# Kernel optimization log

Measured on AMD Instinct MI355X. Metric: run time of the kernel, lower is better.

Reference implementation:

```python
import jax, jax.numpy as jnp
import numpy as np

K = 1024            # atoms per chain
L = 4 * K - 9       # 2*(K-3) sin/cos dihedrals + (K-2) len13 + (K-1) bond lengths
EPS = 1e-6


def _denorm(v, lo, hi):
    # map [-1, 1] -> [lo, hi]
    return (v + 1.0) * 0.5 * (hi - lo) + lo


def _output_arr2values(v):
    # split flat NN output into (sin/cos dihedrals, hedron len13, bond lengths)
    n_d = K - 3
    sc = v[: 2 * n_d].reshape(n_d, 2)                     # (sin, cos) per dihedral
    d13 = _denorm(v[2 * n_d : 2 * n_d + K - 2], 1.5, 5.0)  # 1-3 distances, [1.5, 5]
    bl = _denorm(v[2 * n_d + K - 2 :], 0.9, 3.0)           # bond lengths,  [0.9, 3]
    return sc, d13, bl


def _len2ang(sc, d13, bl):
    # bond angles via law of cosines from consecutive bond lengths + 1-3 distance
    l1, l2 = bl[:-1], bl[1:]
    ct = (l1 * l1 + l2 * l2 - d13 * d13) / (2.0 * l1 * l2)
    theta = jnp.arccos(jnp.clip(ct, -1.0 + EPS, 1.0 - EPS))   # (K-2,) radians
    chi = jnp.arctan2(sc[:, 0], sc[:, 1])                      # (K-3,) radians
    return theta, chi


def _len_ang2coords(bl, theta, chi):
    # sequential NeRF chain extension: place atom i from atoms i-3, i-2, i-1
    a0 = jnp.zeros(3, dtype=bl.dtype)
    a1 = jnp.array([1.0, 0.0, 0.0], dtype=bl.dtype) * bl[0]
    t0 = theta[0]
    a2 = a1 + bl[1] * jnp.stack([-jnp.cos(t0), jnp.sin(t0), jnp.zeros((), bl.dtype)])

    def step(carry, inp):
        a, b, c = carry
        l, th, ch = inp
        bc = c - b
        bc = bc / (jnp.linalg.norm(bc) + EPS)
        n = jnp.cross(b - a, bc)
        n = n / (jnp.linalg.norm(n) + EPS)
        m = jnp.cross(n, bc)
        st = jnp.sin(th)
        d = c + l * (-jnp.cos(th) * bc + st * jnp.cos(ch) * m + st * jnp.sin(ch) * n)
        return (b, c, d), d

    _, rest = jax.lax.scan(step, (a0, a1, a2), (bl[2:], theta[1:], chi))
    return jnp.concatenate([jnp.stack([a0, a1, a2]), rest], axis=0)  # (K, 3)


def _chain2coords(v):
    sc, d13, bl = _output_arr2values(v)
    theta, chi = _len2ang(sc, d13, bl)
    return _len_ang2coords(bl, theta, chi)


def setup_inputs() -> dict:
    key = jax.random.key(0)
    k1, k2 = jax.random.split(key)
    B = 2048
    predictions = 2.0 * jax.random.uniform(k1, (B, L), dtype=jnp.float32) - 1.0
    targets = 2.0 * jax.random.uniform(k2, (B, L), dtype=jnp.float32) - 1.0
    return {"predictions": predictions, "targets": targets}


def reference(predictions, targets):
    p = jnp.clip(predictions, -1.0, 1.0)           # only predictions are clamped
    pred_coords = jax.vmap(_chain2coords)(p)        # (B, K, 3)
    targ_coords = jax.vmap(_chain2coords)(targets)  # (B, K, 3)
    return jnp.mean(jnp.square(pred_coords - targ_coords))
```

## Files before the change

### kernel.cpp

```cpp
#include <hip/hip_runtime.h>


#define LROW  4087
#define NSTEP 1021
#define NROW  2048
#define CHUNK 8
#define EPSF  1e-6f
#define INVMEAN (1.0f / (2048.0f * 1024.0f * 3.0f))

__device__ __forceinline__ float frcp(float x){ return __builtin_amdgcn_rcpf(x); }
__device__ __forceinline__ float frsq(float x){ return __builtin_amdgcn_rsqf(x); }

struct Xf { float f[12]; };

__device__ __forceinline__ Xf xident(){
  Xf X;
  X.f[0]=1.f; X.f[1]=0.f; X.f[2]=0.f;
  X.f[3]=0.f; X.f[4]=1.f; X.f[5]=0.f;
  X.f[6]=0.f; X.f[7]=0.f; X.f[8]=1.f;
  X.f[9]=0.f; X.f[10]=0.f; X.f[11]=0.f;
  return X;
}

__device__ __forceinline__ Xf xcombine(const Xf& A, const Xf& B){
  Xf C;
  #pragma unroll
  for (int c3 = 0; c3 < 12; c3 += 3){
    const float bx = B.f[c3], by = B.f[c3+1], bz = B.f[c3+2];
    C.f[c3]   = A.f[0]*bx + A.f[3]*by + A.f[6]*bz;
    C.f[c3+1] = A.f[1]*bx + A.f[4]*by + A.f[7]*bz;
    C.f[c3+2] = A.f[2]*bx + A.f[5]*by + A.f[8]*bz;
  }
  C.f[9] += A.f[9]; C.f[10] += A.f[10]; C.f[11] += A.f[11];
  return C;
}

__device__ __forceinline__ void xstepP(Xf& X, float Px, float Py, float Pz){
  const float l2 = Px*Px + Py*Py + Pz*Pz;
  const float q  = frsq(l2);
  const float hx = q*Px, hy = q*Py, hz = q*Pz;
  const float ist = frsq(fmaxf(hy*hy + hz*hz, 1e-12f));
  const float ux = X.f[0]*Px + X.f[3]*Py + X.f[6]*Pz;
  const float uy = X.f[1]*Px + X.f[4]*Py + X.f[7]*Pz;
  const float uz = X.f[2]*Px + X.f[5]*Py + X.f[8]*Pz;
  X.f[9] += ux; X.f[10] += uy; X.f[11] += uz;
  const float n0x = q*ux, n0y = q*uy, n0z = q*uz;
  const float n1x = ist*(hx*n0x - X.f[0]);
  const float n1y = ist*(hx*n0y - X.f[1]);
  const float n1z = ist*(hx*n0z - X.f[2]);
  const float n2x = ist*(hy*X.f[6] - hz*X.f[3]);
  const float n2y = ist*(hy*X.f[7] - hz*X.f[4]);
  const float n2z = ist*(hy*X.f[8] - hz*X.f[5]);
  X.f[0]=n0x; X.f[1]=n0y; X.f[2]=n0z;
  X.f[3]=n1x; X.f[4]=n1y; X.f[5]=n1z;
  X.f[6]=n2x; X.f[7]=n2y; X.f[8]=n2z;
}

__device__ __forceinline__ void xinitP(Xf& X, float Px, float Py, float Pz){
  const float l2 = Px*Px + Py*Py + Pz*Pz;
  const float q  = frsq(l2);
  const float hx = q*Px, hy = q*Py, hz = q*Pz;
  const float s2 = fmaxf(hy*hy + hz*hz, 1e-12f);
  const float ist = frsq(s2);
  const float st  = s2 * ist;
  X.f[0]=hx;        X.f[1]=hy;          X.f[2]=hz;
  X.f[3]=-st;       X.f[4]=hx*hy*ist;   X.f[5]=hx*hz*ist;
  X.f[6]=0.f;       X.f[7]=-hz*ist;     X.f[8]=hy*ist;
  X.f[9]=Px;        X.f[10]=Py;        X.f[11]=Pz;
}

__global__ void __launch_bounds__(256, 4)
rmsd_kernel(const float* __restrict__ pred, const float* __restrict__ targ,
            float* __restrict__ ws){
  __shared__ float pos[128*25 + 8];
  __shared__ float Tbuf[2][12];
  __shared__ float ini[3];
  __shared__ float part;

  const int row  = blockIdx.x;
  const int tid  = threadIdx.x;
  const int ln   = tid & 63;
  const int wv   = tid >> 6;
  const int c    = wv >> 1;
  const int half = wv & 1;
  const int lid  = (half << 6) | ln;
  const int j0   = lid * CHUNK;

  const float* __restrict__ v = (c ? targ : pred) + (size_t)row * LROW;
  const float cl = c ? 1e30f : 1.0f;

  const float rb0 = fminf(fmaxf(v[3064], -cl), cl);
  const float rd0 = fminf(fmaxf(v[2042], -cl), cl);
  const float rb1w= fminf(fmaxf(v[3065], -cl), cl);

  float s0[CHUNK], s1[CHUNK], dd[CHUNK], bv[CHUNK+1];
  #pragma unroll
  for (int k = 0; k < CHUNK; ++k){
    s0[k] = v[2*(j0+k)];
    s1[k] = v[2*(j0+k)+1];
    dd[k] = v[2043 + j0 + k];
  }
  #pragma unroll
  for (int m = 0; m <= CHUNK; ++m){
    int ix = 3065 + j0 + m;
    if (ix > 4086) ix = 4086;
    bv[m] = v[ix];
  }
  #pragma unroll
  for (int m = 0; m <= CHUNK; ++m)
    bv[m] = fmaf(fminf(fmaxf(bv[m], -cl), cl), 1.05f, 1.95f);

  float Px[CHUNK], Py[CHUNK], Pz[CHUNK];
  #pragma unroll
  for (int k = 0; k < CHUNK; ++k){
    const float a0 = fminf(fmaxf(s0[k], -cl), cl);
    const float a1 = fminf(fmaxf(s1[k], -cl), cl);
    const float d  = fmaf(fminf(fmaxf(dd[k], -cl), cl), 1.75f, 3.25f);
    const float b1 = bv[k], b2 = bv[k+1];
    float ct = (b1*b1 + b2*b2 - d*d) * frcp(2.0f*b1*b2);
    ct = fminf(fmaxf(ct, -1.0f + EPSF), 1.0f - EPSF);
    const float st = sqrtf(fmaxf(1.0f - ct*ct, 0.0f));
    const float r2 = a0*a0 + a1*a1;
    const bool ok = r2 > 1e-36f;
    const float ir = ok ? frcp(sqrtf(r2)) : 0.0f;
    const float scv = a0 * ir;
    const float ccv = ok ? a1 * ir : 1.0f;
    Px[k] = -b2 * ct;
    Py[k] = b2 * st * ccv;
    Pz[k] = b2 * st * scv;
  }

  Xf X;
  float tl[CHUNK][3];
  xinitP(X, Px[0], Py[0], Pz[0]);
  tl[0][0]=X.f[9]; tl[0][1]=X.f[10]; tl[0][2]=X.f[11];
  #pragma unroll
  for (int k = 1; k < CHUNK; ++k){
    if (j0 + k < NSTEP) xstepP(X, Px[k], Py[k], Pz[k]);
    tl[k][0]=X.f[9]; tl[k][1]=X.f[10]; tl[k][2]=X.f[11];
  }

  #pragma unroll
  for (int off = 1; off < 64; off <<= 1){
    Xf o;
    #pragma unroll
    for (int i = 0; i < 12; ++i) o.f[i] = __shfl_up(X.f[i], off);
    if (ln >= off) X = xcombine(o, X);
  }

  if (half == 0 && ln == 63){
    #pragma unroll
    for (int i = 0; i < 12; ++i) Tbuf[c][i] = X.f[i];
  }

  Xf E;
  #pragma unroll
  for (int i = 0; i < 12; ++i) E.f[i] = __shfl_up(X.f[i], 1);
  if (ln == 0) E = xident();

  __syncthreads();

  if (half == 1){
    Xf T;
    #pragma unroll
    for (int i = 0; i < 12; ++i) T.f[i] = Tbuf[c][i];
    E = xcombine(T, E);
  }

  const float bl0 = fmaf(rb0,  1.05f, 1.95f);
  const float d0  = fmaf(rd0,  1.75f, 3.25f);
  const float b1f = fmaf(rb1w, 1.05f, 1.95f);
  float ct0 = (bl0*bl0 + b1f*b1f - d0*d0) * frcp(2.0f*bl0*b1f);
  ct0 = fminf(fmaxf(ct0, -1.0f + EPSF), 1.0f - EPSF);
  const float st0 = sqrtf(fmaxf(1.0f - ct0*ct0, 0.0f));
  const float a1x = bl0;
  const float a2x = bl0 - b1f*ct0;
  const float a2y = b1f*st0;

  Xf G;
  #pragma unroll
  for (int c3 = 0; c3 < 12; c3 += 3){
    const float ex = E.f[c3], ey = E.f[c3+1], ez = E.f[c3+2];
    G.f[c3]   = -ct0*ex - st0*ey;
    G.f[c3+1] =  st0*ex - ct0*ey;
    G.f[c3+2] =  ez;
  }
  G.f[9] += a2x; G.f[10] += a2y;

  #pragma unroll
  for (int k = 0; k < CHUNK; ++k){
    const float tx = tl[k][0], ty = tl[k][1], tz = tl[k][2];
    tl[k][0] = G.f[9]  + G.f[0]*tx + G.f[3]*ty + G.f[6]*tz;
    tl[k][1] = G.f[10] + G.f[1]*tx + G.f[4]*ty + G.f[7]*tz;
    tl[k][2] = G.f[11] + G.f[2]*tx + G.f[5]*ty + G.f[8]*tz;
  }

  if (c == 0){
    #pragma unroll
    for (int k = 0; k < CHUNK; ++k){
      if (j0 + k < NSTEP){
        const int o = lid*25 + 3*k;
        pos[o] = tl[k][0]; pos[o+1] = tl[k][1]; pos[o+2] = tl[k][2];
      }
    }
    if (lid == 0){ ini[0] = a1x; ini[1] = a2x; ini[2] = a2y; }
  }
  __syncthreads();

  float acc = 0.0f;
  if (c == 1){
    if (lid == 0){
      const float dx = ini[0] - a1x;
      const float dy = ini[1] - a2x;
      const float dz = ini[2] - a2y;
      acc = dx*dx + dy*dy + dz*dz;
    }
    #pragma unroll
    for (int k = 0; k < CHUNK; ++k){
      if (j0 + k < NSTEP){
        const int o = lid*25 + 3*k;
        const float dx = pos[o]   - tl[k][0];
        const float dy = pos[o+1] - tl[k][1];
        const float dz = pos[o+2] - tl[k][2];
        acc = fmaf(dx, dx, acc);
        acc = fmaf(dy, dy, acc);
        acc = fmaf(dz, dz, acc);
      }
    }
    #pragma unroll
    for (int off = 32; off > 0; off >>= 1) acc += __shfl_down(acc, off);
    if (half == 1 && ln == 0) part = acc;
  }
  __syncthreads();
  if (wv == 2 && ln == 0) ws[row] = acc + part;
}

__global__ void __launch_bounds__(256, 1)
reduce_kernel(const float* __restrict__ ws, float* __restrict__ out){
  __shared__ float wsum[4];
  const int tid = threadIdx.x;
  float a = 0.0f;
  #pragma unroll
  for (int i = 0; i < 8; ++i) a += ws[tid + (i << 8)];
  #pragma unroll
  for (int off = 32; off > 0; off >>= 1) a += __shfl_down(a, off);
  if ((tid & 63) == 0) wsum[tid >> 6] = a;
  __syncthreads();
  if (tid == 0) out[0] = (wsum[0] + wsum[1] + wsum[2] + wsum[3]) * INVMEAN;
}

extern "C" void kernel_launch(void* const* d_in, const int* in_sizes, int n_in,
                              void* d_out, int out_size, void* d_ws, size_t ws_size,
                              hipStream_t stream) {
  const float* pred = (const float*)d_in[0];
  const float* targ = (const float*)d_in[1];
  float* out = (float*)d_out;
  float* ws  = (float*)d_ws;

  rmsd_kernel<<<NROW, 256, 0, stream>>>(pred, targ, ws);
  reduce_kernel<<<1, 256, 0, stream>>>(ws, out);
}
```

Baseline: 108.2 us.

## Scan rotations as two frame columns and decouple translation prefix sum

```diff
diff --git a/kernel.cpp b/kernel.cpp
--- a/kernel.cpp
+++ b/kernel.cpp
@@ -10,64 +10,6 @@
 
 __device__ __forceinline__ float frcp(float x){ return __builtin_amdgcn_rcpf(x); }
 __device__ __forceinline__ float frsq(float x){ return __builtin_amdgcn_rsqf(x); }
-
-struct Xf { float f[12]; };
-
-__device__ __forceinline__ Xf xident(){
-  Xf X;
-  X.f[0]=1.f; X.f[1]=0.f; X.f[2]=0.f;
-  X.f[3]=0.f; X.f[4]=1.f; X.f[5]=0.f;
-  X.f[6]=0.f; X.f[7]=0.f; X.f[8]=1.f;
-  X.f[9]=0.f; X.f[10]=0.f; X.f[11]=0.f;
-  return X;
-}
-
-__device__ __forceinline__ Xf xcombine(const Xf& A, const Xf& B){
-  Xf C;
-  #pragma unroll
-  for (int c3 = 0; c3 < 12; c3 += 3){
-    const float bx = B.f[c3], by = B.f[c3+1], bz = B.f[c3+2];
-    C.f[c3]   = A.f[0]*bx + A.f[3]*by + A.f[6]*bz;
-    C.f[c3+1] = A.f[1]*bx + A.f[4]*by + A.f[7]*bz;
-    C.f[c3+2] = A.f[2]*bx + A.f[5]*by + A.f[8]*bz;
-  }
-  C.f[9] += A.f[9]; C.f[10] += A.f[10]; C.f[11] += A.f[11];
-  return C;
-}
-
-__device__ __forceinline__ void xstepP(Xf& X, float Px, float Py, float Pz){
-  const float l2 = Px*Px + Py*Py + Pz*Pz;
-  const float q  = frsq(l2);
-  const float hx = q*Px, hy = q*Py, hz = q*Pz;
-  const float ist = frsq(fmaxf(hy*hy + hz*hz, 1e-12f));
-  const float ux = X.f[0]*Px + X.f[3]*Py + X.f[6]*Pz;
-  const float uy = X.f[1]*Px + X.f[4]*Py + X.f[7]*Pz;
-  const float uz = X.f[2]*Px + X.f[5]*Py + X.f[8]*Pz;
-  X.f[9] += ux; X.f[10] += uy; X.f[11] += uz;
-  const float n0x = q*ux, n0y = q*uy, n0z = q*uz;
-  const float n1x = ist*(hx*n0x - X.f[0]);
-  const float n1y = ist*(hx*n0y - X.f[1]);
-  const float n1z = ist*(hx*n0z - X.f[2]);
-  const float n2x = ist*(hy*X.f[6] - hz*X.f[3]);
-  const float n2y = ist*(hy*X.f[7] - hz*X.f[4]);
-  const float n2z = ist*(hy*X.f[8] - hz*X.f[5]);
-  X.f[0]=n0x; X.f[1]=n0y; X.f[2]=n0z;
-  X.f[3]=n1x; X.f[4]=n1y; X.f[5]=n1z;
-  X.f[6]=n2x; X.f[7]=n2y; X.f[8]=n2z;
-}
-
-__device__ __forceinline__ void xinitP(Xf& X, float Px, float Py, float Pz){
-  const float l2 = Px*Px + Py*Py + Pz*Pz;
-  const float q  = frsq(l2);
-  const float hx = q*Px, hy = q*Py, hz = q*Pz;
-  const float s2 = fmaxf(hy*hy + hz*hz, 1e-12f);
-  const float ist = frsq(s2);
-  const float st  = s2 * ist;
-  X.f[0]=hx;        X.f[1]=hy;          X.f[2]=hz;
-  X.f[3]=-st;       X.f[4]=hx*hy*ist;   X.f[5]=hx*hz*ist;
-  X.f[6]=0.f;       X.f[7]=-hz*ist;     X.f[8]=hy*ist;
-  X.f[9]=Px;        X.f[10]=Py;        X.f[11]=Pz;
-}
 
 __global__ void __launch_bounds__(256, 4)
 rmsd_kernel(const float* __restrict__ pred, const float* __restrict__ targ,
@@ -110,7 +52,8 @@
   for (int m = 0; m <= CHUNK; ++m)
     bv[m] = fmaf(fminf(fmaxf(bv[m], -cl), cl), 1.05f, 1.95f);
 
-  float Px[CHUNK], Py[CHUNK], Pz[CHUNK];
+  float c0x,c0y,c0z, c1x,c1y,c1z, c2x,c2y,c2z, tx,ty,tz;
+  float tl[CHUNK][3];
   #pragma unroll
   for (int k = 0; k < CHUNK; ++k){
     const float a0 = fminf(fmaxf(s0[k], -cl), cl);
@@ -119,52 +62,102 @@
     const float b1 = bv[k], b2 = bv[k+1];
     float ct = (b1*b1 + b2*b2 - d*d) * frcp(2.0f*b1*b2);
     ct = fminf(fmaxf(ct, -1.0f + EPSF), 1.0f - EPSF);
-    const float st = sqrtf(fmaxf(1.0f - ct*ct, 0.0f));
+    const float omc = fmaxf(1.0f - ct*ct, 1e-12f);
+    const float ist = frsq(omc);
+    const float st  = omc * ist;
     const float r2 = a0*a0 + a1*a1;
     const bool ok = r2 > 1e-36f;
-    const float ir = ok ? frcp(sqrtf(r2)) : 0.0f;
+    const float ir = ok ? frsq(r2) : 0.0f;
     const float scv = a0 * ir;
     const float ccv = ok ? a1 * ir : 1.0f;
-    Px[k] = -b2 * ct;
-    Py[k] = b2 * st * ccv;
-    Pz[k] = b2 * st * scv;
-  }
-
-  Xf X;
-  float tl[CHUNK][3];
-  xinitP(X, Px[0], Py[0], Pz[0]);
-  tl[0][0]=X.f[9]; tl[0][1]=X.f[10]; tl[0][2]=X.f[11];
-  #pragma unroll
-  for (int k = 1; k < CHUNK; ++k){
-    if (j0 + k < NSTEP) xstepP(X, Px[k], Py[k], Pz[k]);
-    tl[k][0]=X.f[9]; tl[k][1]=X.f[10]; tl[k][2]=X.f[11];
-  }
-
+    const float hx = -ct, hy = st*ccv, hz = st*scv;
+    if (k == 0){
+      c0x=hx;      c0y=hy;      c0z=hz;
+      c1x=-st;     c1y=hx*ccv;  c1z=hx*scv;
+      c2x=0.0f;    c2y=-scv;    c2z=ccv;
+      tx=b2*hx;    ty=b2*hy;    tz=b2*hz;
+    } else {
+      const float n0x = c0x*hx + c1x*hy + c2x*hz;
+      const float n0y = c0y*hx + c1y*hy + c2y*hz;
+      const float n0z = c0z*hx + c1z*hy + c2z*hz;
+      tx = fmaf(b2, n0x, tx); ty = fmaf(b2, n0y, ty); tz = fmaf(b2, n0z, tz);
+      const float n1x = ist * fmaf(hx, n0x, -c0x);
+      const float n1y = ist * fmaf(hx, n0y, -c0y);
+      const float n1z = ist * fmaf(hx, n0z, -c0z);
+      const float n2x = fmaf(ccv, c2x, -scv*c1x);
+      const float n2y = fmaf(ccv, c2y, -scv*c1y);
+      const float n2z = fmaf(ccv, c2z, -scv*c1z);
+      c0x=n0x; c0y=n0y; c0z=n0z;
+      c1x=n1x; c1y=n1y; c1z=n1z;
+      c2x=n2x; c2y=n2y; c2z=n2z;
+    }
+    tl[k][0]=tx; tl[k][1]=ty; tl[k][2]=tz;
+  }
+
+  float r0x=c0x, r0y=c0y, r0z=c0z, r1x=c1x, r1y=c1y, r1z=c1z;
   #pragma unroll
   for (int off = 1; off < 64; off <<= 1){
-    Xf o;
-    #pragma unroll
-    for (int i = 0; i < 12; ++i) o.f[i] = __shfl_up(X.f[i], off);
-    if (ln >= off) X = xcombine(o, X);
-  }
-
-  if (half == 0 && ln == 63){
-    #pragma unroll
-    for (int i = 0; i < 12; ++i) Tbuf[c][i] = X.f[i];
-  }
-
-  Xf E;
-  #pragma unroll
-  for (int i = 0; i < 12; ++i) E.f[i] = __shfl_up(X.f[i], 1);
-  if (ln == 0) E = xident();
-
+    const float o0x=__shfl_up(r0x,off), o0y=__shfl_up(r0y,off), o0z=__shfl_up(r0z,off);
+    const float o1x=__shfl_up(r1x,off), o1y=__shfl_up(r1y,off), o1z=__shfl_up(r1z,off);
+    const float o2x = o0y*o1z - o0z*o1y;
+    const float o2y = o0z*o1x - o0x*o1z;
+    const float o2z = o0x*o1y - o0y*o1x;
+    const float n0x = o0x*r0x + o1x*r0y + o2x*r0z;
+    const float n0y = o0y*r0x + o1y*r0y + o2y*r0z;
+    const float n0z = o0z*r0x + o1z*r0y + o2z*r0z;
+    const float n1x = o0x*r1x + o1x*r1y + o2x*r1z;
+    const float n1y = o0y*r1x + o1y*r1y + o2y*r1z;
+    const float n1z = o0z*r1x + o1z*r1y + o2z*r1z;
+    if (ln >= off){
+      r0x=n0x; r0y=n0y; r0z=n0z;
+      r1x=n1x; r1y=n1y; r1z=n1z;
+    }
+  }
+
+  float e0x=__shfl_up(r0x,1), e0y=__shfl_up(r0y,1), e0z=__shfl_up(r0z,1);
+  float e1x=__shfl_up(r1x,1), e1y=__shfl_up(r1y,1), e1z=__shfl_up(r1z,1);
+  if (ln == 0){ e0x=1.f; e0y=0.f; e0z=0.f; e1x=0.f; e1y=1.f; e1z=0.f; }
+
+  {
+    const float x2x = e0y*e1z - e0z*e1y;
+    const float x2y = e0z*e1x - e0x*e1z;
+    const float x2z = e0x*e1y - e0y*e1x;
+    const float wx = e0x*tx + e1x*ty + x2x*tz;
+    const float wy = e0y*tx + e1y*ty + x2y*tz;
+    const float wz = e0z*tx + e1z*ty + x2z*tz;
+    float sx=wx, sy=wy, sz=wz;
+    #pragma unroll
+    for (int off = 1; off < 64; off <<= 1){
+      const float ax=__shfl_up(sx,off), ay=__shfl_up(sy,off), az=__shfl_up(sz,off);
+      if (ln >= off){ sx+=ax; sy+=ay; sz+=az; }
+    }
+    tx = sx - wx; ty = sy - wy; tz = sz - wz;
+
+    if (half == 0 && ln == 63){
+      Tbuf[c][0]=r0x; Tbuf[c][1]=r0y; Tbuf[c][2]=r0z;
+      Tbuf[c][3]=r1x; Tbuf[c][4]=r1y; Tbuf[c][5]=r1z;
+      Tbuf[c][6]=sx;  Tbuf[c][7]=sy;  Tbuf[c][8]=sz;
+    }
+  }
   __syncthreads();
 
   if (half == 1){
-    Xf T;
-    #pragma unroll
-    for (int i = 0; i < 12; ++i) T.f[i] = Tbuf[c][i];
-    E = xcombine(T, E);
+    const float T0x=Tbuf[c][0], T0y=Tbuf[c][1], T0z=Tbuf[c][2];
+    const float T1x=Tbuf[c][3], T1y=Tbuf[c][4], T1z=Tbuf[c][5];
+    const float T2x = T0y*T1z - T0z*T1y;
+    const float T2y = T0z*T1x - T0x*T1z;
+    const float T2z = T0x*T1y - T0y*T1x;
+    const float f0x = T0x*e0x + T1x*e0y + T2x*e0z;
+    const float f0y = T0y*e0x + T1y*e0y + T2y*e0z;
+    const float f0z = T0z*e0x + T1z*e0y + T2z*e0z;
+    const float f1x = T0x*e1x + T1x*e1y + T2x*e1z;
+    const float f1y = T0y*e1x + T1y*e1y + T2y*e1z;
+    const float f1z = T0z*e1x + T1z*e1y + T2z*e1z;
+    const float ntx = Tbuf[c][6] + T0x*tx + T1x*ty + T2x*tz;
+    const float nty = Tbuf[c][7] + T0y*tx + T1y*ty + T2y*tz;
+    const float ntz = Tbuf[c][8] + T0z*tx + T1z*ty + T2z*tz;
+    e0x=f0x; e0y=f0y; e0z=f0z; e1x=f1x; e1y=f1y; e1z=f1z;
+    tx=ntx; ty=nty; tz=ntz;
   }
 
   const float bl0 = fmaf(rb0,  1.05f, 1.95f);
@@ -177,22 +170,23 @@
   const float a2x = bl0 - b1f*ct0;
   const float a2y = b1f*st0;
 
-  Xf G;
-  #pragma unroll
-  for (int c3 = 0; c3 < 12; c3 += 3){
-    const float ex = E.f[c3], ey = E.f[c3+1], ez = E.f[c3+2];
-    G.f[c3]   = -ct0*ex - st0*ey;
-    G.f[c3+1] =  st0*ex - ct0*ey;
-    G.f[c3+2] =  ez;
-  }
-  G.f[9] += a2x; G.f[10] += a2y;
+  const float e2x = e0y*e1z - e0z*e1y;
+  const float e2y = e0z*e1x - e0x*e1z;
+  const float e2z = e0x*e1y - e0y*e1x;
+
+  const float g0x = -ct0*e0x - st0*e0y, g0y = st0*e0x - ct0*e0y, g0z = e0z;
+  const float g1x = -ct0*e1x - st0*e1y, g1y = st0*e1x - ct0*e1y, g1z = e1z;
+  const float g2x = -ct0*e2x - st0*e2y, g2y = st0*e2x - ct0*e2y, g2z = e2z;
+  const float gtx = a2x - ct0*tx - st0*ty;
+  const float gty = a2y + st0*tx - ct0*ty;
+  const float gtz = tz;
 
   #pragma unroll
   for (int k = 0; k < CHUNK; ++k){
-    const float tx = tl[k][0], ty = tl[k][1], tz = tl[k][2];
-    tl[k][0] = G.f[9]  + G.f[0]*tx + G.f[3]*ty + G.f[6]*tz;
-    tl[k][1] = G.f[10] + G.f[1]*tx + G.f[4]*ty + G.f[7]*tz;
-    tl[k][2] = G.f[11] + G.f[2]*tx + G.f[5]*ty + G.f[8]*tz;
+    const float ux = tl[k][0], uy = tl[k][1], uz = tl[k][2];
+    tl[k][0] = gtx + g0x*ux + g1x*uy + g2x*uz;
+    tl[k][1] = gty + g0y*ux + g1y*uy + g2y*uz;
+    tl[k][2] = gtz + g0z*ux + g1z*uy + g2z*uz;
   }
 
   if (c == 0){
```

Result: faster. 102.1 us (-5.6%).
